# Kernel optimization log

Measured on AMD Instinct MI355X. Metric: run time of the kernel, lower is better.

## Reference

```python
import jax, jax.numpy as jnp
import numpy as np
import math

B, T, C, NH = 8, 1024, 768, 12
HD = C // NH
EPS = 1e-5

def layer_norm(x, g, b):
    mu = jnp.mean(x, axis=-1, keepdims=True)
    var = jnp.mean(jnp.square(x - mu), axis=-1, keepdims=True)
    return (x - mu) * jax.lax.rsqrt(var + EPS) * g + b

def setup_inputs() -> dict:
    key = jax.random.key(0)
    ks = jax.random.split(key, 10)
    s = lambda n: 1.0 / math.sqrt(n)
    return {
        "x": jax.random.normal(ks[0], (B, T, C), jnp.float32),
        "attn_mask": jax.random.randint(ks[1], (B, T), 0, 2, jnp.int32),
        "ln1_g": jnp.ones((C,), jnp.float32),
        "ln1_b": jnp.zeros((C,), jnp.float32),
        "W_attn": jax.random.normal(ks[2], (C, 3 * C), jnp.float32) * s(C),
        "b_attn": jnp.zeros((3 * C,), jnp.float32),
        "W_proj": jax.random.normal(ks[3], (C, C), jnp.float32) * s(C),
        "b_proj": jnp.zeros((C,), jnp.float32),
        "ln2_g": jnp.ones((C,), jnp.float32),
        "ln2_b": jnp.zeros((C,), jnp.float32),
        "W_fc": jax.random.normal(ks[4], (C, 4 * C), jnp.float32) * s(C),
        "b_fc": jnp.zeros((4 * C,), jnp.float32),
        "W_fc2": jax.random.normal(ks[5], (4 * C, C), jnp.float32) * s(4 * C),
        "b_fc2": jnp.zeros((C,), jnp.float32),
    }

def reference(x, attn_mask, ln1_g, ln1_b, W_attn, b_attn, W_proj, b_proj,
              ln2_g, ln2_b, W_fc, b_fc, W_fc2, b_fc2):
    # --- attention branch ---
    h = layer_norm(x, ln1_g, ln1_b)                     # [B,T,C]
    qkv = h @ W_attn + b_attn                           # [B,T,3C]
    q, k, v = jnp.split(qkv, 3, axis=-1)
    q = q.reshape(B, T, NH, HD).transpose(0, 2, 1, 3)   # [B,H,T,D]
    k = k.reshape(B, T, NH, HD).transpose(0, 2, 1, 3)
    v = v.reshape(B, T, NH, HD).transpose(0, 2, 1, 3)
    attn = jnp.einsum('bhqd,bhkd->bhqk', q, k) * (1.0 / math.sqrt(HD))
    mask = attn_mask[:, None, None, :]                  # [B,1,1,T] key-padding
    attn = jnp.where(mask == 0, -jnp.inf, attn)
    attn = jax.nn.softmax(attn, axis=-1)
    o = jnp.einsum('bhqk,bhkd->bhqd', attn, v)          # [B,H,T,D]
    o = o.transpose(0, 2, 1, 3).reshape(B, T, C)
    x = x + (o @ W_proj + b_proj)
    # --- MLP branch ---
    h2 = layer_norm(x, ln2_g, ln2_b)
    h2 = jax.nn.gelu(h2 @ W_fc + b_fc, approximate=True)
    x = x + (h2 @ W_fc2 + b_fc2)
    return x
```

## Files before the change

kernel.cpp:

```cpp
#include <hip/hip_runtime.h>
#include <hip/hip_bf16.h>
#include <math.h>

constexpr int kB  = 8;
constexpr int kT  = 1024;
constexpr int kC  = 768;
constexpr int kNH = 12;
constexpr int kHD = 64;
constexpr int kM  = kB * kT;
constexpr int k3C = 3 * kC;
constexpr int k4C = 4 * kC;

typedef __bf16 bf16x8 __attribute__((ext_vector_type(8)));
typedef float  f32x4  __attribute__((ext_vector_type(4)));
typedef unsigned short u16x8 __attribute__((ext_vector_type(8)));

__device__ inline void gload_lds16(const void* g, void* l) {
  __builtin_amdgcn_global_load_lds(
      (const __attribute__((address_space(1))) void*)g,
      (__attribute__((address_space(3))) void*)l, 16, 0, 0);
}

__device__ inline float ldx(const float* p) { return *p; }
__device__ inline float ldx(const __hip_bfloat16* p) { return __bfloat162float(*p); }

template <typename TIN>
__global__ __launch_bounds__(256) void ln_kernel(
    const TIN* __restrict__ x, const float* __restrict__ g,
    const float* __restrict__ bta, __hip_bfloat16* __restrict__ out)
{
  __shared__ float red[4];
  int row = blockIdx.x;
  int tid = threadIdx.x;
  const TIN* xr = x + (size_t)row * kC;
  float v0 = ldx(xr + tid), v1 = ldx(xr + tid + 256), v2 = ldx(xr + tid + 512);

  float s = v0 + v1 + v2;
#pragma unroll
  for (int off = 32; off; off >>= 1) s += __shfl_xor(s, off);
  if ((tid & 63) == 0) red[tid >> 6] = s;
  __syncthreads();
  float mu = (red[0] + red[1] + red[2] + red[3]) * (1.0f / kC);

  float d0 = v0 - mu, d1 = v1 - mu, d2 = v2 - mu;
  float q = d0 * d0 + d1 * d1 + d2 * d2;
#pragma unroll
  for (int off = 32; off; off >>= 1) q += __shfl_xor(q, off);
  __syncthreads();
  if ((tid & 63) == 0) red[tid >> 6] = q;
  __syncthreads();
  float var = (red[0] + red[1] + red[2] + red[3]) * (1.0f / kC);
  float inv = rsqrtf(var + 1e-5f);

  __hip_bfloat16* orow = out + (size_t)row * kC;
  orow[tid]       = __float2bfloat16(d0 * inv * g[tid]       + bta[tid]);
  orow[tid + 256] = __float2bfloat16(d1 * inv * g[tid + 256] + bta[tid + 256]);
  orow[tid + 512] = __float2bfloat16(d2 * inv * g[tid + 512] + bta[tid + 512]);
}

__global__ __launch_bounds__(256) void transpose_cast(
    const float* __restrict__ W, __hip_bfloat16* __restrict__ WT, int K, int N)
{
  __shared__ __hip_bfloat16 t[64][65];
  int k0 = blockIdx.y * 64, n0 = blockIdx.x * 64;
  int tid = threadIdx.x;
#pragma unroll
  for (int it = 0; it < 16; ++it) {
    int e = it * 256 + tid;
    int r = e >> 6, c = e & 63;
    t[r][c] = __float2bfloat16(W[(size_t)(k0 + r) * N + n0 + c]);
  }
  __syncthreads();
#pragma unroll
  for (int it = 0; it < 16; ++it) {
    int e = it * 256 + tid;
    int nr = e >> 6, kc = e & 63;
    WT[(size_t)(n0 + nr) * K + k0 + kc] = t[kc][nr];
  }
}

__global__ __launch_bounds__(256) void v_transpose(
    const __hip_bfloat16* __restrict__ qkv, __hip_bfloat16* __restrict__ vt)
{
  __shared__ __hip_bfloat16 tile[64][80];
  int b = blockIdx.z, h = blockIdx.y, t0 = blockIdx.x * 64;
  int tid = threadIdx.x;
  const __hip_bfloat16* vb = qkv + (size_t)(b * kT) * k3C + 2 * kC + h * kHD;
#pragma unroll
  for (int it = 0; it < 2; ++it) {
    int e = it * 256 + tid;
    int r = e >> 3, c8 = (e & 7) * 8;
    *(u16x8*)&tile[r][c8] = *(const u16x8*)(vb + (size_t)(t0 + r) * k3C + c8);
  }
  __syncthreads();
  __hip_bfloat16* vrow = vt + (size_t)(b * kNH + h) * kHD * kT;
#pragma unroll
  for (int it = 0; it < 2; ++it) {
    int e = it * 256 + tid;
    int d = e >> 3, k8 = (e & 7) * 8;
    u16x8 u;
#pragma unroll
    for (int m = 0; m < 8; ++m)
      u[m] = *(const unsigned short*)&tile[k8 + m][d];
    *(u16x8*)(vrow + (size_t)d * kT + t0 + k8) = u;
  }
}

__device__ inline float gelu_fast(float c) {
  float t = 0.7978845608028654f * (c + 0.044715f * c * c * c);
  float e = exp2f(t * 2.8853900817779268f);
  float th = 1.0f - 2.0f * __builtin_amdgcn_rcpf(e + 1.0f);
  return 0.5f * c * (1.0f + th);
}

template <int MODE>
__global__ __launch_bounds__(256) void gemm_bf16(
    const __hip_bfloat16* __restrict__ A,
    const __hip_bfloat16* __restrict__ WT,
    const float* __restrict__ bias,
    const void* __restrict__ Rv,
    void* __restrict__ outv, int M, int N, int K)
{
  __shared__ __align__(16) __hip_bfloat16 As[2][128 * 64];
  __shared__ __align__(16) __hip_bfloat16 Bs[2][128 * 64];
  const int tid  = threadIdx.x;
  const int lane = tid & 63, wid = tid >> 6;
  const int wr = wid >> 1, wc = wid & 1;
  const int r16 = lane & 15, g = lane >> 4;

  const int nwg = gridDim.x * gridDim.y;
  const int bid = blockIdx.y * gridDim.x + blockIdx.x;
  const int swz = (bid & 7) * (nwg >> 3) + (bid >> 3);
  const int m0 = (swz / gridDim.x) * 128;
  const int n0 = (swz % gridDim.x) * 128;

  const __hip_bfloat16* Abase = A  + (size_t)m0 * K;
  const __hip_bfloat16* Bbase = WT + (size_t)n0 * K;

  f32x4 acc[4][4] = {};

  auto stage = [&](int t, int buf) {
    const __hip_bfloat16* Ap = Abase + t * 64;
    const __hip_bfloat16* Bp = Bbase + t * 64;
#pragma unroll
    for (int it = 0; it < 4; ++it) {
      int e = it * 256 + tid;
      int row = e >> 3, ch = (e & 7) ^ (row & 7);
      char* la = (char*)&As[buf][0] + (it * 4096 + (tid & ~63) * 16);
      char* lb = (char*)&Bs[buf][0] + (it * 4096 + (tid & ~63) * 16);
      gload_lds16(Ap + (size_t)row * K + ch * 8, la);
      gload_lds16(Bp + (size_t)row * K + ch * 8, lb);
    }
  };

  auto compute = [&](const char* Ab, const char* Bb) {
#pragma unroll
    for (int s = 0; s < 2; ++s) {
      bf16x8 af[4], bf[4];
#pragma unroll
      for (int i = 0; i < 4; ++i) {
        int ar = wr * 64 + i * 16 + r16;
        af[i] = *(const bf16x8*)(Ab + ar * 128 + (((s * 4 + g) ^ (ar & 7)) << 4));
        int br = wc * 64 + i * 16 + r16;
        bf[i] = *(const bf16x8*)(Bb + br * 128 + (((s * 4 + g) ^ (br & 7)) << 4));
      }
#pragma unroll
      for (int i = 0; i < 4; ++i)
#pragma unroll
        for (int j = 0; j < 4; ++j)
          acc[i][j] = __builtin_amdgcn_mfma_f32_16x16x32_bf16(af[i], bf[j],
                                                              acc[i][j], 0, 0, 0);
    }
  };

  const int NT = K >> 6;
  stage(0, 0);
  __syncthreads();

  for (int t = 0; t < NT; t += 2) {
    stage(t + 1, 1);
    compute((const char*)&As[0][0], (const char*)&Bs[0][0]);
    __syncthreads();
    if (t + 2 < NT) stage(t + 2, 0);
    compute((const char*)&As[1][0], (const char*)&Bs[1][0]);
    __syncthreads();
  }

  const int r0 = m0 + wr * 64 + g * 4;
  const int c0 = n0 + wc * 64 + r16;
#pragma unroll
  for (int i = 0; i < 4; ++i) {
#pragma unroll
    for (int j = 0; j < 4; ++j) {
      int col = c0 + j * 16;
      float bv = bias[col];
#pragma unroll
      for (int q = 0; q < 4; ++q) {
        int row = r0 + i * 16 + q;
        float c = acc[i][j][q] + bv;
        if (MODE == 3) {
          c += ((const float*)Rv)[(size_t)row * N + col];
          ((__hip_bfloat16*)outv)[(size_t)row * N + col] = __float2bfloat16(c);
        } else if (MODE == 4) {
          c += __bfloat162float(((const __hip_bfloat16*)Rv)[(size_t)row * N + col]);
          ((float*)outv)[(size_t)row * N + col] = c;
        } else {
          if (MODE == 2) c = gelu_fast(c);
          ((__hip_bfloat16*)outv)[(size_t)row * N + col] = __float2bfloat16(c);
        }
      }
    }
  }
}

__global__ __launch_bounds__(256) void attn_mfma(
    const __hip_bfloat16* __restrict__ qkv,
    const __hip_bfloat16* __restrict__ vt,
    const int* __restrict__ mask,
    __hip_bfloat16* __restrict__ o)
{
  __shared__ __align__(16) __hip_bfloat16 Ks[64 * 64];
  __shared__ __align__(16) __hip_bfloat16 Vs[64 * 64];
  __shared__ __align__(16) __hip_bfloat16 Ps[4 * 16 * 64];

  const int b = blockIdx.z, h = blockIdx.y, q0 = blockIdx.x * 64;
  const int tid = threadIdx.x, lane = tid & 63, wid = tid >> 6;
  const int r16 = lane & 15, g = lane >> 4;
  const size_t rs = k3C;
  const __hip_bfloat16* qb = qkv + (size_t)(b * kT) * rs + h * kHD;
  const __hip_bfloat16* kb = qb + kC;
  const __hip_bfloat16* vtb = vt + (size_t)(b * kNH + h) * kHD * kT;
  const int* mrow = mask + b * kT;
  constexpr float kSc = 0.125f * 1.4426950408889634f;

  bf16x8 qf[2];
  {
    const __hip_bfloat16* qr = qb + (size_t)(q0 + wid * 16 + r16) * rs;
#pragma unroll
    for (int s = 0; s < 2; ++s) qf[s] = *(const bf16x8*)(qr + s * 32 + g * 8);
  }

  f32x4 o_acc[4] = {};
  float l_part[4] = {0.f, 0.f, 0.f, 0.f};

  __hip_bfloat16* Pw = Ps + wid * 1024;

  for (int t = 0; t < 16; ++t) {
    __syncthreads();
#pragma unroll
    for (int it = 0; it < 2; ++it) {
      int e = it * 256 + tid;
      int row = e >> 3, ch = (e & 7) ^ (row & 7);
      char* lk = (char*)Ks + (it * 4096 + (tid & ~63) * 16);
      char* lv = (char*)Vs + (it * 4096 + (tid & ~63) * 16);
      gload_lds16(kb + (size_t)(t * 64 + row) * rs + ch * 8, lk);
      gload_lds16(vtb + (size_t)row * kT + t * 64 + ch * 8, lv);
    }
    __syncthreads();

    f32x4 sa[4] = {};
#pragma unroll
    for (int j = 0; j < 4; ++j) {
#pragma unroll
      for (int s = 0; s < 2; ++s) {
        int kr = 16 * j + r16;
        bf16x8 kf = *(const bf16x8*)((const char*)Ks + kr * 128 +
                                     (((s * 4 + g) ^ (kr & 7)) << 4));
        sa[j] = __builtin_amdgcn_mfma_f32_16x16x32_bf16(qf[s], kf, sa[j], 0, 0, 0);
      }
    }

    float keep[4];
#pragma unroll
    for (int j = 0; j < 4; ++j)
      keep[j] = (mrow[t * 64 + 16 * j + r16] != 0) ? 1.f : 0.f;

#pragma unroll
    for (int r = 0; r < 4; ++r) {
      float p[4];
#pragma unroll
      for (int j = 0; j < 4; ++j)
        p[j] = keep[j] != 0.f ? exp2f(sa[j][r] * kSc) : 0.f;
      l_part[r] += (p[0] + p[1]) + (p[2] + p[3]);
      int q = g * 4 + r;
      char* pwq = (char*)Pw + q * 128 + (r16 & 7) * 2;
#pragma unroll
      for (int j = 0; j < 4; ++j) {
        int chn = ((j << 1) | (r16 >> 3)) ^ (q & 7);
        *(__hip_bfloat16*)(pwq + (chn << 4)) = __float2bfloat16(p[j]);
      }
    }

    asm volatile("s_waitcnt lgkmcnt(0)" ::: "memory");
    __builtin_amdgcn_sched_barrier(0);

#pragma unroll
    for (int s = 0; s < 2; ++s) {
      bf16x8 pf = *(const bf16x8*)((const char*)Pw + r16 * 128 +
                                   (((s * 4 + g) ^ (r16 & 7)) << 4));
#pragma unroll
      for (int db = 0; db < 4; ++db) {
        int vr = 16 * db + r16;
        bf16x8 vf = *(const bf16x8*)((const char*)Vs + vr * 128 +
                                     (((s * 4 + g) ^ (vr & 7)) << 4));
        o_acc[db] = __builtin_amdgcn_mfma_f32_16x16x32_bf16(pf, vf, o_acc[db], 0, 0, 0);
      }
    }
  }

#pragma unroll
  for (int r = 0; r < 4; ++r) {
    float l = l_part[r];
#pragma unroll
    for (int off = 8; off; off >>= 1) l += __shfl_xor(l, off);
    float inv = 1.f / l;
    size_t row = (size_t)(b * kT) + q0 + wid * 16 + g * 4 + r;
#pragma unroll
    for (int db = 0; db < 4; ++db)
      o[row * kC + h * kHD + 16 * db + r16] = __float2bfloat16(o_acc[db][r] * inv);
  }
}

extern "C" void kernel_launch(void* const* d_in, const int* in_sizes, int n_in,
                              void* d_out, int out_size, void* d_ws, size_t ws_size,
                              hipStream_t stream) {
  const float* x      = (const float*)d_in[0];
  const int*   amask  = (const int*)  d_in[1];
  const float* ln1_g  = (const float*)d_in[2];
  const float* ln1_b  = (const float*)d_in[3];
  const float* W_attn = (const float*)d_in[4];
  const float* b_attn = (const float*)d_in[5];
  const float* W_proj = (const float*)d_in[6];
  const float* b_proj = (const float*)d_in[7];
  const float* ln2_g  = (const float*)d_in[8];
  const float* ln2_b  = (const float*)d_in[9];
  const float* W_fc   = (const float*)d_in[10];
  const float* b_fc   = (const float*)d_in[11];
  const float* W_fc2  = (const float*)d_in[12];
  const float* b_fc2  = (const float*)d_in[13];
  float* out = (float*)d_out;

  char* ws = (char*)d_ws;
  __hip_bfloat16* h_bf    = (__hip_bfloat16*)(ws);
  __hip_bfloat16* qkv_bf  = (__hip_bfloat16*)(ws + (size_t)16 * 1024 * 1024);
  __hip_bfloat16* fc_bf   = qkv_bf;
  __hip_bfloat16* wt_attn = (__hip_bfloat16*)(ws + (size_t)68 * 1024 * 1024);
  __hip_bfloat16* wt_proj = (__hip_bfloat16*)(ws + (size_t)72 * 1024 * 1024);
  __hip_bfloat16* wt_fc   = (__hip_bfloat16*)(ws + (size_t)74 * 1024 * 1024);
  __hip_bfloat16* wt_fc2  = (__hip_bfloat16*)(ws + (size_t)79 * 1024 * 1024);
  __hip_bfloat16* vt_bf   = (__hip_bfloat16*)(ws + (size_t)84 * 1024 * 1024);
  __hip_bfloat16* x1_bf   = vt_bf;

  dim3 blk(256);

  transpose_cast<<<dim3(k3C / 64, kC / 64), blk, 0, stream>>>(W_attn, wt_attn, kC, k3C);
  transpose_cast<<<dim3(kC / 64, kC / 64), blk, 0, stream>>>(W_proj, wt_proj, kC, kC);
  transpose_cast<<<dim3(k4C / 64, kC / 64), blk, 0, stream>>>(W_fc, wt_fc, kC, k4C);
  transpose_cast<<<dim3(kC / 64, k4C / 64), blk, 0, stream>>>(W_fc2, wt_fc2, k4C, kC);

  ln_kernel<float><<<kM, blk, 0, stream>>>(x, ln1_g, ln1_b, h_bf);
  gemm_bf16<0><<<dim3(k3C / 128, kM / 128), blk, 0, stream>>>(
      h_bf, wt_attn, b_attn, nullptr, qkv_bf, kM, k3C, kC);
  v_transpose<<<dim3(kT / 64, kNH, kB), blk, 0, stream>>>(qkv_bf, vt_bf);
  attn_mfma<<<dim3(kT / 64, kNH, kB), blk, 0, stream>>>(qkv_bf, vt_bf, amask, h_bf);
  gemm_bf16<3><<<dim3(kC / 128, kM / 128), blk, 0, stream>>>(
      h_bf, wt_proj, b_proj, x, x1_bf, kM, kC, kC);
  ln_kernel<__hip_bfloat16><<<kM, blk, 0, stream>>>(x1_bf, ln2_g, ln2_b, h_bf);
  gemm_bf16<2><<<dim3(k4C / 128, kM / 128), blk, 0, stream>>>(
      h_bf, wt_fc, b_fc, nullptr, fc_bf, kM, k4C, kC);
  gemm_bf16<4><<<dim3(kC / 128, kM / 128), blk, 0, stream>>>(
      fc_bf, wt_fc2, b_fc2, x1_bf, out, kM, kC, k4C);
}
```

Measured before the change: 285.7 us.

## Double-buffer K/V tiles in attention and precompute key mask bitmask

The attention kernel now keeps two LDS buffers for K and V. It issues the async global-to-LDS load of the next key tile before computing on the current one, and uses one barrier per iteration instead of two. The key-padding mask is read once per lane into a 64-bit bitmask, which removes the per-tile global mask loads from the inner loop. The costs are twice the LDS for K/V, which may lower occupancy, and exp2 now being evaluated for masked keys too.

```diff
diff --git a/kernel.cpp b/kernel.cpp
--- a/kernel.cpp
+++ b/kernel.cpp
@@ -219,8 +219,8 @@
     const int* __restrict__ mask,
     __hip_bfloat16* __restrict__ o)
 {
-  __shared__ __align__(16) __hip_bfloat16 Ks[64 * 64];
-  __shared__ __align__(16) __hip_bfloat16 Vs[64 * 64];
+  __shared__ __align__(16) __hip_bfloat16 Ks[2][64 * 64];
+  __shared__ __align__(16) __hip_bfloat16 Vs[2][64 * 64];
   __shared__ __align__(16) __hip_bfloat16 Ps[4 * 16 * 64];
 
   const int b = blockIdx.z, h = blockIdx.y, q0 = blockIdx.x * 64;
@@ -233,30 +233,44 @@
   const int* mrow = mask + b * kT;
   constexpr float kSc = 0.125f * 1.4426950408889634f;
 
+  auto stage = [&](int t, int buf) {
+#pragma unroll
+    for (int it = 0; it < 2; ++it) {
+      int e = it * 256 + tid;
+      int row = e >> 3, ch = (e & 7) ^ (row & 7);
+      char* lk = (char*)&Ks[buf][0] + (it * 4096 + (tid & ~63) * 16);
+      char* lv = (char*)&Vs[buf][0] + (it * 4096 + (tid & ~63) * 16);
+      gload_lds16(kb + (size_t)(t * 64 + row) * rs + ch * 8, lk);
+      gload_lds16(vtb + (size_t)row * kT + t * 64 + ch * 8, lv);
+    }
+  };
+
   bf16x8 qf[2];
   {
     const __hip_bfloat16* qr = qb + (size_t)(q0 + wid * 16 + r16) * rs;
 #pragma unroll
     for (int s = 0; s < 2; ++s) qf[s] = *(const bf16x8*)(qr + s * 32 + g * 8);
   }
+  stage(0, 0);
+  unsigned long long km = 0;
+#pragma unroll
+  for (int t = 0; t < 16; ++t)
+#pragma unroll
+    for (int j = 0; j < 4; ++j)
+      if (mrow[t * 64 + 16 * j + r16] != 0)
+        km |= 1ull << (t * 4 + j);
+  __syncthreads();
 
   f32x4 o_acc[4] = {};
   float l_part[4] = {0.f, 0.f, 0.f, 0.f};
-
   __hip_bfloat16* Pw = Ps + wid * 1024;
 
   for (int t = 0; t < 16; ++t) {
-    __syncthreads();
-#pragma unroll
-    for (int it = 0; it < 2; ++it) {
-      int e = it * 256 + tid;
-      int row = e >> 3, ch = (e & 7) ^ (row & 7);
-      char* lk = (char*)Ks + (it * 4096 + (tid & ~63) * 16);
-      char* lv = (char*)Vs + (it * 4096 + (tid & ~63) * 16);
-      gload_lds16(kb + (size_t)(t * 64 + row) * rs + ch * 8, lk);
-      gload_lds16(vtb + (size_t)row * kT + t * 64 + ch * 8, lv);
-    }
-    __syncthreads();
+    const int buf = t & 1;
+    if (t + 1 < 16) stage(t + 1, buf ^ 1);
+
+    const char* Kb = (const char*)&Ks[buf][0];
+    const char* Vb = (const char*)&Vs[buf][0];
 
     f32x4 sa[4] = {};
 #pragma unroll
@@ -264,23 +278,20 @@
 #pragma unroll
       for (int s = 0; s < 2; ++s) {
         int kr = 16 * j + r16;
-        bf16x8 kf = *(const bf16x8*)((const char*)Ks + kr * 128 +
+        bf16x8 kf = *(const bf16x8*)(Kb + kr * 128 +
                                      (((s * 4 + g) ^ (kr & 7)) << 4));
         sa[j] = __builtin_amdgcn_mfma_f32_16x16x32_bf16(qf[s], kf, sa[j], 0, 0, 0);
       }
     }
 
-    float keep[4];
-#pragma unroll
-    for (int j = 0; j < 4; ++j)
-      keep[j] = (mrow[t * 64 + 16 * j + r16] != 0) ? 1.f : 0.f;
-
 #pragma unroll
     for (int r = 0; r < 4; ++r) {
       float p[4];
 #pragma unroll
-      for (int j = 0; j < 4; ++j)
-        p[j] = keep[j] != 0.f ? exp2f(sa[j][r] * kSc) : 0.f;
+      for (int j = 0; j < 4; ++j) {
+        float pj = exp2f(sa[j][r] * kSc);
+        p[j] = ((km >> (t * 4 + j)) & 1ull) ? pj : 0.f;
+      }
       l_part[r] += (p[0] + p[1]) + (p[2] + p[3]);
       int q = g * 4 + r;
       char* pwq = (char*)Pw + q * 128 + (r16 & 7) * 2;
@@ -301,11 +312,12 @@
 #pragma unroll
       for (int db = 0; db < 4; ++db) {
         int vr = 16 * db + r16;
-        bf16x8 vf = *(const bf16x8*)((const char*)Vs + vr * 128 +
+        bf16x8 vf = *(const bf16x8*)(Vb + vr * 128 +
                                      (((s * 4 + g) ^ (vr & 7)) << 4));
         o_acc[db] = __builtin_amdgcn_mfma_f32_16x16x32_bf16(pf, vf, o_acc[db], 0, 0, 0);
       }
     }
+    __syncthreads();
   }
 
 #pragma unroll
```

After: 287.0 us. Within noise of the previous version (+0.4%).
